# Performance work log

Measured on AMD Instinct MI355X. Metric: run time of the kernel, lower is better.

## Reference

```python
import jax, jax.numpy as jnp
import numpy as np

BATCH, SEQ, DIM = 4, 4096, 256
DT_RANK, D_STATE, NUM_TOKENS = 16, 16, 1024


def _adapool(x, T):
    # uniform window mean == AdaptiveAvgPool1d when S % T == 0
    B, S, D = x.shape
    return x.reshape(B, T, S // T, D).mean(axis=2)


def _layernorm(x, g, b, eps=1e-5):
    mu = x.mean(-1, keepdims=True)
    var = ((x - mu) ** 2).mean(-1, keepdims=True)
    return (x - mu) * jax.lax.rsqrt(var + eps) * g + b


def _gauss_mask(T):
    c = (T + 1) // 2
    idx = jnp.arange(T, dtype=jnp.float32)
    sigma = jnp.abs(idx - c).mean()
    w = jnp.exp(-0.5 * (idx - c) ** 2 / sigma ** 2)
    return w / w.sum()


def _ssm(x, Wdbc, Wdt, bdt, Alog, D):
    A = -jnp.exp(Alog)                                     # (Dm, N)
    dbc = x @ Wdbc.T                                       # (B,L,dt+2N)
    delta = jax.nn.softplus(dbc[..., :DT_RANK] @ Wdt.T + bdt)   # (B,L,Dm)
    Bm = dbc[..., DT_RANK:DT_RANK + D_STATE]               # (B,L,N)
    Cm = dbc[..., DT_RANK + D_STATE:]                      # (B,L,N)
    deltaA = jnp.exp(delta[..., None] * A)                 # (B,L,Dm,N)
    BX = (delta[..., None] * Bm[:, :, None, :]) * x[..., None]
    def comb(c1, c2):
        a1, x1 = c1
        a2, x2 = c2
        return (a2 * a1, a2 * x1 + x2)
    _, hs = jax.lax.associative_scan(comb, (deltaA, BX), axis=1)
    y = jnp.einsum('bldn,bln->bld', hs, Cm) + D * x
    return y


def setup_inputs():
    key = jax.random.key(0)
    ks = jax.random.split(key, 16)
    s = 0.05
    Alog = jnp.tile(jnp.log(jnp.arange(1.0, D_STATE + 1.0, dtype=jnp.float32))[None, :], (DIM, 1))
    return {
        'x': jax.random.normal(ks[0], (BATCH, SEQ, DIM), jnp.float32),
        'ln_g': jnp.ones((DIM,), jnp.float32),
        'ln_b': jnp.zeros((DIM,), jnp.float32),
        'W1': jax.random.normal(ks[1], (DIM, DIM), jnp.float32) * s,
        'b1': jnp.zeros((DIM,), jnp.float32),
        'W2': jax.random.normal(ks[2], (DIM, DIM), jnp.float32) * s,
        'b2': jnp.zeros((DIM,), jnp.float32),
        'Wcf': jax.random.normal(ks[3], (DIM, DIM), jnp.float32) * s,
        'bcf': jnp.zeros((DIM,), jnp.float32),
        'Wcb': jax.random.normal(ks[4], (DIM, DIM), jnp.float32) * s,
        'bcb': jnp.zeros((DIM,), jnp.float32),
        'Wdbc_f': jax.random.normal(ks[5], (DT_RANK + 2 * D_STATE, DIM), jnp.float32) * s,
        'Wdt_f': jax.random.normal(ks[6], (DIM, DT_RANK), jnp.float32) * s,
        'bdt_f': jnp.zeros((DIM,), jnp.float32),
        'Alog_f': Alog,
        'D_f': jnp.ones((DIM,), jnp.float32),
        'Wdbc_b': jax.random.normal(ks[7], (DT_RANK + 2 * D_STATE, DIM), jnp.float32) * s,
        'Wdt_b': jax.random.normal(ks[8], (DIM, DT_RANK), jnp.float32) * s,
        'bdt_b': jnp.zeros((DIM,), jnp.float32),
        'Alog_b': Alog,
        'D_b': jnp.ones((DIM,), jnp.float32),
    }


def reference(x, ln_g, ln_b, W1, b1, W2, b2, Wcf, bcf, Wcb, bcb,
              Wdbc_f, Wdt_f, bdt_f, Alog_f, D_f,
              Wdbc_b, Wdt_b, bdt_b, Alog_b, D_b):
    skip = _adapool(x, NUM_TOKENS)
    xn = _layernorm(x, ln_g, ln_b)
    z = xn @ W1.T + b1
    xp = xn @ W2.T + b2
    mask = _gauss_mask(NUM_TOKENS)[None, :, None]

    # forward direction: 1x1 conv (= channel linear) -> softplus -> SSM
    h1 = jax.nn.softplus(jnp.einsum('bsd,ed->bse', xp, Wcf) + bcf)
    x1 = _ssm(h1, Wdbc_f, Wdt_f, bdt_f, Alog_f, D_f)
    x1 = jax.nn.silu(_adapool(x1, NUM_TOKENS) * mask)

    # backward direction on flipped sequence
    h2 = jax.nn.softplus(jnp.einsum('bsd,ed->bse', xp[:, ::-1], Wcb) + bcb)
    x2 = _ssm(h2, Wdbc_b, Wdt_b, bdt_b, Alog_b, D_b)[:, ::-1]
    x2 = jax.nn.silu(_adapool(x2, NUM_TOKENS) * mask)

    zp = jax.nn.silu(_adapool(z, NUM_TOKENS))
    return zp * x1 + zp * x2 + skip
```

## Files before the change

kernel.cpp:

```cpp
#include <hip/hip_runtime.h>
#include <math.h>


namespace {
constexpr int BB = 4;
constexpr int LL = 4096;
constexpr int DD = 256;
constexpr int NS = 16;
constexpr int NCH = 128;
constexpr int CLEN = 32;
constexpr int NG  = CLEN / 8;
constexpr int TOK = 1024;

constexpr size_t NROW = (size_t)BB * LL;
constexpr size_t NE   = NROW * DD;
constexpr size_t NP   = (size_t)BB * TOK * DD;
constexpr size_t NBC  = NROW * NS;
constexpr size_t NAGG = 2ull * BB * DD * NCH * NS;
constexpr size_t NSD  = 2ull * BB * NCH * DD;

constexpr size_t O_H1X  = 0;
constexpr size_t O_G2X  = NE / 2;
constexpr size_t O_H1T  = NE;
constexpr size_t O_G2T  = NE + NE / 2;
constexpr size_t O_DLTF = 2 * NE;
constexpr size_t O_XN   = O_DLTF;
constexpr size_t O_DLTB = 2 * NE + NE / 2;
constexpr size_t O_BMF  = 3 * NE;
constexpr size_t O_CMF  = O_BMF + NBC / 2;
constexpr size_t O_BMB  = O_CMF + NBC / 2;
constexpr size_t O_CMB  = O_BMB + NBC / 2;
constexpr size_t O_ZP   = O_CMB + NBC / 2;
constexpr size_t O_WF1  = O_ZP + NP;
constexpr size_t O_BF1  = O_WF1 + 768 * 256 / 2;
constexpr size_t O_WF2F = O_BF1 + 768;
constexpr size_t O_B2F  = O_WF2F + 384 * 256 / 2;
constexpr size_t O_WF2B = O_B2F + 384;
constexpr size_t O_B2B  = O_WF2B + 384 * 256 / 2;
constexpr size_t O_SD   = O_B2B + 384;
constexpr size_t O_HEND = O_SD + NSD;
constexpr size_t O_HIN  = O_HEND + NAGG / 2;
constexpr size_t O_MASK = O_HIN + NAGG / 2;

constexpr int SST = 136;
constexpr int NWPREP = 1282;
}

typedef __bf16 bf16x8 __attribute__((ext_vector_type(8)));
typedef __bf16 bf16x4 __attribute__((ext_vector_type(4)));
typedef float f32x4 __attribute__((ext_vector_type(4)));

__device__ __forceinline__ float softplusf(float x) {
    return fmaxf(x, 0.f) + __logf(1.f + __expf(-fabsf(x)));
}
__device__ __forceinline__ float siluf(float x) {
    return x / (1.f + __expf(-x));
}
__device__ __forceinline__ void gl_lds16(const void* g, void* l) {
    __builtin_amdgcn_global_load_lds((const __attribute__((address_space(1))) unsigned int*)g,
                                     (__attribute__((address_space(3))) unsigned int*)l, 16, 0, 0);
}
__device__ __forceinline__ int st_addr(int col, int row) {
    return col * SST + ((((row >> 3) ^ (col >> 3)) & 15) << 3) + (row & 7);
}
__device__ __forceinline__ void pow_chain(float e1, float* p) {
    p[0] = e1;
    p[1] = e1 * e1;
    p[2] = p[1] * e1;
    p[3] = p[1] * p[1];
    p[4] = p[3] * p[0];
    p[5] = p[3] * p[1];
    p[6] = p[3] * p[2];
    p[7] = p[3] * p[3];
    p[8]  = p[7] * p[0];
    p[9]  = p[7] * p[1];
    p[10] = p[7] * p[2];
    p[11] = p[7] * p[3];
    p[12] = p[7] * p[4];
    p[13] = p[7] * p[5];
    p[14] = p[7] * p[6];
    p[15] = p[7] * p[7];
}

#define GEMM_KLOOP(SHBASE, GA, GB, WR, WC, WV, LANE, ACC)                          \
    {                                                                               \
        _Pragma("unroll")                                                           \
        for (int rg = 0; rg < 2; ++rg) {                                            \
            gl_lds16((GA) + rg * 16 * 256, &(SHBASE)[((WV) * 2 + rg) * 512]);       \
            gl_lds16((GB) + rg * 16 * 256, &(SHBASE)[4096 + ((WV) * 2 + rg) * 512]);\
        }                                                                           \
        _Pragma("unroll")                                                           \
        for (int kst = 0; kst < 8; ++kst) {                                         \
            if (kst < 7) {                                                          \
                __bf16* Asn = (SHBASE) + ((kst + 1) & 1) * 8192;                    \
                int k0n = (kst + 1) * 32;                                           \
                _Pragma("unroll")                                                   \
                for (int rg = 0; rg < 2; ++rg) {                                    \
                    gl_lds16((GA) + rg * 16 * 256 + k0n, &Asn[((WV) * 2 + rg) * 512]);      \
                    gl_lds16((GB) + rg * 16 * 256 + k0n, &Asn[4096 + ((WV) * 2 + rg) * 512]);\
                }                                                                   \
                asm volatile("s_waitcnt vmcnt(4)" ::: "memory");                    \
            } else {                                                                \
                asm volatile("s_waitcnt vmcnt(0)" ::: "memory");                    \
            }                                                                       \
            __builtin_amdgcn_s_barrier();                                           \
            __builtin_amdgcn_sched_barrier(0);                                      \
            const __bf16* Ac = (SHBASE) + (kst & 1) * 8192;                         \
            const __bf16* Bc = Ac + 4096;                                           \
            bf16x8 af[4], bfr[4];                                                   \
            _Pragma("unroll")                                                       \
            for (int i = 0; i < 4; ++i)                                             \
                af[i] = *(const bf16x8*)&Ac[((WR) * 4 + i) * 512 + (LANE) * 8];     \
            _Pragma("unroll")                                                       \
            for (int j = 0; j < 4; ++j)                                             \
                bfr[j] = *(const bf16x8*)&Bc[((WC) * 4 + j) * 512 + (LANE) * 8];    \
            _Pragma("unroll")                                                       \
            for (int i = 0; i < 4; ++i)                                             \
                _Pragma("unroll")                                                   \
                for (int j = 0; j < 4; ++j)                                         \
                    ACC[i][j] = __builtin_amdgcn_mfma_f32_16x16x32_bf16(af[i], bfr[j], ACC[i][j], 0, 0, 0); \
            __builtin_amdgcn_s_barrier();                                           \
        }                                                                           \
    }

__global__ __launch_bounds__(256) void prep_ln_kernel(
    const float* __restrict__ x, const float* __restrict__ lng, const float* __restrict__ lnb,
    const float* __restrict__ W1, const float* __restrict__ b1,
    const float* __restrict__ W2, const float* __restrict__ b2,
    const float* __restrict__ Wcf, const float* __restrict__ bcf,
    const float* __restrict__ Wcb, const float* __restrict__ bcb,
    const float* __restrict__ Wdt_f, const float* __restrict__ Wdbc_f, const float* __restrict__ bdt_f,
    const float* __restrict__ Wdt_b, const float* __restrict__ Wdbc_b, const float* __restrict__ bdt_b,
    __bf16* __restrict__ xn, float* __restrict__ outp,
    __bf16* __restrict__ Wf1, float* __restrict__ bf1,
    __bf16* __restrict__ Wf2f, float* __restrict__ b2f,
    __bf16* __restrict__ Wf2b, float* __restrict__ b2b,
    float* __restrict__ mask)
{
    int bxg = blockIdx.x;
    int k = threadIdx.x;
    if (bxg >= NWPREP) {
        __shared__ float ls[4][256];
        int r0 = (bxg - NWPREP) * 4;
        int w = k >> 6, l = k & 63;
        int row = r0 + w;
        float4 v = *(const float4*)&x[(size_t)row * 256 + l * 4];
        float s = v.x + v.y + v.z + v.w;
        float q = v.x * v.x + v.y * v.y + v.z * v.z + v.w * v.w;
        for (int o = 32; o > 0; o >>= 1) {
            s += __shfl_xor(s, o, 64);
            q += __shfl_xor(q, o, 64);
        }
        float mu = s * (1.f / 256.f);
        float rs = rsqrtf(q * (1.f / 256.f) - mu * mu + 1e-5f);
        float4 g4 = *(const float4*)&lng[l * 4];
        float4 b4 = *(const float4*)&lnb[l * 4];
        bf16x4 o4;
        o4[0] = (__bf16)((v.x - mu) * rs * g4.x + b4.x);
        o4[1] = (__bf16)((v.y - mu) * rs * g4.y + b4.y);
        o4[2] = (__bf16)((v.z - mu) * rs * g4.z + b4.z);
        o4[3] = (__bf16)((v.w - mu) * rs * g4.w + b4.w);
        *(bf16x4*)&xn[(size_t)row * 256 + l * 4] = o4;
        *(float4*)&ls[w][l * 4] = v;
        __syncthreads();
        int b = r0 >> 12;
        int g = (r0 & 4095) >> 2;
        float acc = ls[0][k] + ls[1][k] + ls[2][k] + ls[3][k];
        outp[((size_t)b * TOK + g) * 256 + k] = acc * 0.25f;
        return;
    }
    int j2 = bxg;
    int mat = j2 / 641;
    int bx = j2 % 641;
    if (bx < 256) {
        int j = bx;
        const float* Wc = mat ? Wcb : Wcf;
        float acc = 0.f, accb = 0.f;
#pragma unroll 8
        for (int m = 0; m < 256; ++m) {
            float w = Wc[j * 256 + m];
            acc  = fmaf(w, W2[m * 256 + k], acc);
            accb = fmaf(w, b2[m], accb);
        }
        Wf1[(size_t)(256 + mat * 256 + j) * 256 + k] = (__bf16)acc;
        if (k == 0) bf1[256 + mat * 256 + j] = accb + (mat ? bcb[j] : bcf[j]);
        if (mat == 0) {
            Wf1[(size_t)j * 256 + k] = (__bf16)W1[j * 256 + k];
            if (k == 0) bf1[j] = b1[j];
        }
    } else if (bx < 640) {
        int j = bx - 256;
        const float* Wdt  = mat ? Wdt_b : Wdt_f;
        const float* Wdbc = mat ? Wdbc_b : Wdbc_f;
        const float* bdt  = mat ? bdt_b : bdt_f;
        __bf16* Wf2 = mat ? Wf2b : Wf2f;
        float* b2x  = mat ? b2b : b2f;
        float val;
        if (j < 256) {
            float acc = 0.f;
#pragma unroll
            for (int m = 0; m < 16; ++m)
                acc = fmaf(Wdt[j * 16 + m], Wdbc[m * 256 + k], acc);
            val = acc;
        } else if (j < 288) {
            val = Wdbc[(16 + (j - 256)) * 256 + k];
        } else {
            val = 0.f;
        }
        Wf2[(size_t)j * 256 + k] = (__bf16)val;
        if (k == 0) b2x[j] = (j < 256) ? bdt[j] : 0.f;
    } else if (mat == 0) {
        __shared__ float red2[4];
        __shared__ float sb;
        float w[4];
        float loc = 0.f;
#pragma unroll
        for (int q = 0; q < 4; ++q) {
            float dd = (float)(k + 256 * q) - 512.f;
            w[q] = __expf(-0.5f * dd * dd * (1.f / 65536.f));
            loc += w[q];
        }
        for (int o = 32; o > 0; o >>= 1) loc += __shfl_xor(loc, o, 64);
        if ((k & 63) == 0) red2[k >> 6] = loc;
        __syncthreads();
        if (k == 0) sb = red2[0] + red2[1] + red2[2] + red2[3];
        __syncthreads();
        float inv = 1.f / sb;
#pragma unroll
        for (int q = 0; q < 4; ++q) mask[k + 256 * q] = w[q] * inv;
    }
}

__global__ __launch_bounds__(256) void gemm1_mfma(
    const __bf16* __restrict__ A, const __bf16* __restrict__ Bw, const float* __restrict__ bias,
    float* __restrict__ zp, __bf16* __restrict__ h1x, __bf16* __restrict__ g2x,
    __bf16* __restrict__ h1T, __bf16* __restrict__ g2T)
{
    __shared__ __align__(16) __bf16 SH[128 * SST];
    int tid = threadIdx.x;
    int lane = tid & 63, wv = tid >> 6;
    int wr = wv >> 1, wc = wv & 1;
    int lm = lane & 15, lq = lane >> 4;
    int m0 = blockIdx.x << 7, n0 = blockIdx.y << 7;

    const __bf16* gaB = A  + (size_t)(m0 + wv * 32 + lm) * 256 + lq * 8;
    const __bf16* gbB = Bw + (size_t)(n0 + wv * 32 + lm) * 256 + lq * 8;

    f32x4 acc[4][4];
#pragma unroll
    for (int i = 0; i < 4; ++i)
#pragma unroll
        for (int j = 0; j < 4; ++j) acc[i][j] = 0;

    GEMM_KLOOP(SH, gaB, gbB, wr, wc, wv, lane, acc)

    int target = blockIdx.y >> 1;
    int colbase = (blockIdx.y & 1) * 128;
    __syncthreads();
    if (target == 0) {
        float* zs = (float*)SH;
#pragma unroll
        for (int j = 0; j < 4; ++j) {
            int coll = wc * 64 + j * 16 + lm;
            float bv = bias[n0 + coll];
#pragma unroll
            for (int i = 0; i < 4; ++i) {
                int gl = wr * 16 + i * 4 + lq;
                float s = acc[i][j][0] + acc[i][j][1] + acc[i][j][2] + acc[i][j][3];
                zs[gl * 132 + coll] = siluf(0.25f * s + bv);
            }
        }
        __syncthreads();
        int b = m0 >> 12, g0 = (m0 & 4095) >> 2;
        int rl = tid >> 5;
        int c4 = (tid & 31) * 4;
#pragma unroll
        for (int p = 0; p < 4; ++p) {
            int g = p * 8 + rl;
            float4 v = *(float4*)&zs[g * 132 + c4];
            *(float4*)&zp[((size_t)b * TOK + g0 + g) * 256 + colbase + c4] = v;
        }
    } else {
        __bf16* hs = SH;
#pragma unroll
        for (int j = 0; j < 4; ++j) {
            int coll = wc * 64 + j * 16 + lm;
            float bv = bias[n0 + coll];
#pragma unroll
            for (int i = 0; i < 4; ++i) {
                int rl = wr * 64 + i * 16 + lq * 4;
                bf16x4 v4;
#pragma unroll
                for (int r = 0; r < 4; ++r)
                    v4[r] = (__bf16)softplusf(acc[i][j][r] + bv);
                *(bf16x4*)&hs[st_addr(coll, rl)] = v4;
            }
        }
        __syncthreads();
        __bf16* outp = (target == 1) ? h1x : g2x;
        __bf16* outT = (target == 1) ? h1T : g2T;
        {
            int tg = tid >> 4;
#pragma unroll
            for (int it = 0; it < 8; ++it) {
                int dcol = it * 16 + (tid & 15);
                bf16x8 v = *(const bf16x8*)&hs[dcol * SST + (((tg ^ (dcol >> 3)) & 15) << 3)];
                *(bf16x8*)&outT[(((size_t)(m0 >> 3) + tg) * 256 + colbase + dcol) * 8] = v;
            }
        }
        {
            int rl2 = tid >> 4;
            int c8 = (tid & 15) * 8;
#pragma unroll
            for (int p = 0; p < 8; ++p) {
                int row = p * 16 + rl2;
                bf16x8 v;
#pragma unroll
                for (int e = 0; e < 8; ++e) v[e] = hs[st_addr(c8 + e, row)];
                *(bf16x8*)&outp[(size_t)(m0 + row) * 256 + colbase + c8] = v;
            }
        }
    }
}

__global__ __launch_bounds__(256) void gemm2_mfma(
    const __bf16* __restrict__ h1x, const __bf16* __restrict__ g2x,
    const __bf16* __restrict__ Wf, const float* __restrict__ bf2,
    const __bf16* __restrict__ Wb, const float* __restrict__ bb2,
    __bf16* __restrict__ dTf, __bf16* __restrict__ dTb,
    __bf16* __restrict__ BmF, __bf16* __restrict__ CmF,
    __bf16* __restrict__ BmB, __bf16* __restrict__ CmB)
{
    __shared__ __align__(16) __bf16 SH[128 * SST];
    int tid = threadIdx.x;
    int lane = tid & 63, wv = tid >> 6;
    int wr = wv >> 1, wc = wv & 1;
    int lm = lane & 15, lq = lane >> 4;
    int m0 = blockIdx.x << 7, n0 = blockIdx.y << 7;
    int dir = blockIdx.z;
    const __bf16* A    = dir ? g2x : h1x;
    const __bf16* Bw   = dir ? Wb : Wf;
    const float* bias  = dir ? bb2 : bf2;
    __bf16* dT = dir ? dTb : dTf;
    __bf16* Bm = dir ? BmB : BmF;
    __bf16* Cm = dir ? CmB : CmF;

    const __bf16* gaB = A  + (size_t)(m0 + wv * 32 + lm) * 256 + lq * 8;
    const __bf16* gbB = Bw + (size_t)(n0 + wv * 32 + lm) * 256 + lq * 8;

    f32x4 acc[4][4];
#pragma unroll
    for (int i = 0; i < 4; ++i)
#pragma unroll
        for (int j = 0; j < 4; ++j) acc[i][j] = 0;

    GEMM_KLOOP(SH, gaB, gbB, wr, wc, wv, lane, acc)

    __syncthreads();
    if (blockIdx.y < 2) {
        __bf16* hs = SH;
        int colbase = blockIdx.y * 128;
#pragma unroll
        for (int j = 0; j < 4; ++j) {
            int coll = wc * 64 + j * 16 + lm;
            float bv = bias[n0 + coll];
#pragma unroll
            for (int i = 0; i < 4; ++i) {
                int rl = wr * 64 + i * 16 + lq * 4;
                bf16x4 v4;
#pragma unroll
                for (int r = 0; r < 4; ++r)
                    v4[r] = (__bf16)softplusf(acc[i][j][r] + bv);
                *(bf16x4*)&hs[st_addr(coll, rl)] = v4;
            }
        }
        __syncthreads();
        int tg = tid >> 4;
#pragma unroll
        for (int it = 0; it < 8; ++it) {
            int dcol = it * 16 + (tid & 15);
            bf16x8 v = *(const bf16x8*)&hs[dcol * SST + (((tg ^ (dcol >> 3)) & 15) << 3)];
            *(bf16x8*)&dT[(((size_t)(m0 >> 3) + tg) * 256 + colbase + dcol) * 8] = v;
        }
    } else {
        __bf16* bs_ = SH;
        __bf16* cs_ = SH + 128 * 24;
        if (wc == 0) {
#pragma unroll
            for (int j = 0; j < 2; ++j) {
                int coll = j * 16 + lm;
                float bv = bias[n0 + coll];
                __bf16* dst = j ? cs_ : bs_;
#pragma unroll
                for (int i = 0; i < 4; ++i) {
                    int rl = wr * 64 + i * 16 + lq * 4;
#pragma unroll
                    for (int r = 0; r < 4; ++r)
                        dst[(rl + r) * 24 + lm] = (__bf16)(acc[i][j][r] + bv);
                }
            }
        }
        __syncthreads();
        int row = tid >> 1;
        int c8 = (tid & 1) * 8;
        bf16x8 vb = *(bf16x8*)&bs_[row * 24 + c8];
        bf16x8 vc = *(bf16x8*)&cs_[row * 24 + c8];
        *(bf16x8*)&Bm[(size_t)(m0 + row) * 16 + c8] = vb;
        *(bf16x8*)&Cm[(size_t)(m0 + row) * 16 + c8] = vc;
    }
}

__global__ __launch_bounds__(256) void scan1_kernel(
    const __bf16* __restrict__ dTf, const __bf16* __restrict__ dTb,
    const __bf16* __restrict__ xTf, const __bf16* __restrict__ xTb,
    const __bf16* __restrict__ bmf, const __bf16* __restrict__ bmb,
    const float* __restrict__ alogf, const float* __restrict__ alogb,
    float* __restrict__ sdb, __bf16* __restrict__ hend)
{
    int d = threadIdx.x;
    int c = blockIdx.x, b = blockIdx.y, dir = blockIdx.z;
    const __bf16* dT = dir ? dTb : dTf;
    const __bf16* xT = dir ? xTb : xTf;
    const __bf16* Bm = dir ? bmb : bmf;
    const float* Alog = dir ? alogb : alogf;

    float A[16];
    bool intOK = true;
#pragma unroll
    for (int n = 0; n < 16; ++n) {
        A[n] = -__expf(Alog[(size_t)d * 16 + n]);
        intOK = intOK && (fabsf(A[n] + (float)(n + 1)) < 1e-3f);
    }
    float h[16];
#pragma unroll
    for (int n = 0; n < 16; ++n) h[n] = 0.f;
    float sd = 0.f;
    size_t rg0 = (size_t)b * 512 + (size_t)c * NG;
    size_t rowb = (size_t)b * LL + (size_t)c * CLEN;
    if (intOK) {
        for (int g = 0; g < NG; ++g) {
            int gg = dir ? (NG - 1 - g) : g;
            size_t ti = ((rg0 + gg) * 256 + d) * 8;
            bf16x8 dv = *(const bf16x8*)&dT[ti];
            bf16x8 xv8 = *(const bf16x8*)&xT[ti];
#pragma unroll
            for (int ii = 0; ii < 8; ++ii) {
                int i = dir ? (7 - ii) : ii;
                float dlt = (float)dv[i];
                float xv  = (float)xv8[i];
                float common = dlt * xv;
                sd += dlt;
                float p[16];
                pow_chain(__expf(-dlt), p);
                const bf16x8* Bp = (const bf16x8*)&Bm[(rowb + gg * 8 + i) * NS];
                bf16x8 b0 = Bp[0], b1 = Bp[1];
#pragma unroll
                for (int n = 0; n < 8; ++n) {
                    h[n]     = fmaf(p[n],     h[n],     common * (float)b0[n]);
                    h[n + 8] = fmaf(p[n + 8], h[n + 8], common * (float)b1[n]);
                }
            }
        }
    } else {
        for (int g = 0; g < NG; ++g) {
            int gg = dir ? (NG - 1 - g) : g;
            size_t ti = ((rg0 + gg) * 256 + d) * 8;
            bf16x8 dv = *(const bf16x8*)&dT[ti];
            bf16x8 xv8 = *(const bf16x8*)&xT[ti];
#pragma unroll
            for (int ii = 0; ii < 8; ++ii) {
                int i = dir ? (7 - ii) : ii;
                float dlt = (float)dv[i];
                float xv  = (float)xv8[i];
                float common = dlt * xv;
                sd += dlt;
                const bf16x8* Bp = (const bf16x8*)&Bm[(rowb + gg * 8 + i) * NS];
                bf16x8 b0 = Bp[0], b1 = Bp[1];
#pragma unroll
                for (int n = 0; n < 8; ++n) {
                    h[n]     = fmaf(__expf(dlt * A[n]),     h[n],     common * (float)b0[n]);
                    h[n + 8] = fmaf(__expf(dlt * A[n + 8]), h[n + 8], common * (float)b1[n]);
                }
            }
        }
    }
    size_t sbase = (size_t)(dir * 4 + b) * NCH + c;
    sdb[sbase * 256 + d] = sd;
    size_t hb = sbase * 16 * 256 + d;
#pragma unroll
    for (int n = 0; n < 16; ++n) hend[hb + (size_t)n * 256] = (__bf16)h[n];
}

__global__ __launch_bounds__(128) void scan2_kernel(
    const float* __restrict__ sdb, const __bf16* __restrict__ hend,
    const float* __restrict__ alogf, const float* __restrict__ alogb,
    __bf16* __restrict__ hin)
{
    int blk = blockIdx.x >> 1;
    int n = blk & 15, b = (blk >> 4) & 3, dir = blk >> 6;
    int d = ((blockIdx.x & 1) << 7) + threadIdx.x;
    const float* Alog = dir ? alogb : alogf;
    float A_dn = -__expf(Alog[(size_t)d * 16 + n]);
    size_t basec = (size_t)(dir * 4 + b) * NCH;
    float s = 0.f;
    if (!dir) {
#pragma unroll 8
        for (int c = 0; c < NCH; ++c) {
            float sdv = sdb[(basec + c) * 256 + d];
            size_t idx = ((basec + c) * 16 + n) * 256 + d;
            float he = (float)hend[idx];
            hin[idx] = (__bf16)s;
            s = fmaf(__expf(sdv * A_dn), s, he);
        }
    } else {
#pragma unroll 8
        for (int c = NCH - 1; c >= 0; --c) {
            float sdv = sdb[(basec + c) * 256 + d];
            size_t idx = ((basec + c) * 16 + n) * 256 + d;
            float he = (float)hend[idx];
            hin[idx] = (__bf16)s;
            s = fmaf(__expf(sdv * A_dn), s, he);
        }
    }
}

__global__ __launch_bounds__(256) void scan3_kernel(
    const __bf16* __restrict__ dTf, const __bf16* __restrict__ dTb,
    const __bf16* __restrict__ xTf, const __bf16* __restrict__ xTb,
    const __bf16* __restrict__ bmf, const __bf16* __restrict__ bmb,
    const __bf16* __restrict__ cmf, const __bf16* __restrict__ cmb,
    const float* __restrict__ alogf, const float* __restrict__ alogb,
    const float* __restrict__ Dfp, const float* __restrict__ Dbp,
    const __bf16* __restrict__ hin,
    const float* __restrict__ zp, const float* __restrict__ mask,
    float* __restrict__ outp)
{
    int d = threadIdx.x;
    int c = blockIdx.x, b = blockIdx.y, dir = blockIdx.z;
    const __bf16* dT = dir ? dTb : dTf;
    const __bf16* xT = dir ? xTb : xTf;
    const __bf16* Bm = dir ? bmb : bmf;
    const __bf16* Cm = dir ? cmb : cmf;
    const float* Alog = dir ? alogb : alogf;
    const float* Dv   = dir ? Dbp : Dfp;

    float A[16];
    bool intOK = true;
#pragma unroll
    for (int n = 0; n < 16; ++n) {
        A[n] = -__expf(Alog[(size_t)d * 16 + n]);
        intOK = intOK && (fabsf(A[n] + (float)(n + 1)) < 1e-3f);
    }
    float Dd = Dv[d];
    float h[16];
    size_t hb = ((size_t)(dir * 4 + b) * NCH + c) * 16 * 256 + d;
#pragma unroll
    for (int n = 0; n < 16; ++n) h[n] = (float)hin[hb + (size_t)n * 256];

    size_t rg0 = (size_t)b * 512 + (size_t)c * NG;
    size_t rowb = (size_t)b * LL + (size_t)c * CLEN;
    int base = c * CLEN;
    float pool = 0.f;
    if (intOK) {
        for (int g = 0; g < NG; ++g) {
            int gg = dir ? (NG - 1 - g) : g;
            size_t ti = ((rg0 + gg) * 256 + d) * 8;
            bf16x8 dv = *(const bf16x8*)&dT[ti];
            bf16x8 xv8 = *(const bf16x8*)&xT[ti];
#pragma unroll
            for (int ii = 0; ii < 8; ++ii) {
                int i = dir ? (7 - ii) : ii;
                float dlt = (float)dv[i];
                float xv  = (float)xv8[i];
                float common = dlt * xv;
                float p[16];
                pow_chain(__expf(-dlt), p);
                size_t row = rowb + gg * 8 + i;
                const bf16x8* Bp = (const bf16x8*)&Bm[row * NS];
                const bf16x8* Cp = (const bf16x8*)&Cm[row * NS];
                bf16x8 b0 = Bp[0], b1 = Bp[1];
                bf16x8 c0 = Cp[0], c1 = Cp[1];
                float yac = 0.f;
#pragma unroll
                for (int n = 0; n < 8; ++n) {
                    h[n]     = fmaf(p[n],     h[n],     common * (float)b0[n]);
                    h[n + 8] = fmaf(p[n + 8], h[n + 8], common * (float)b1[n]);
                    yac = fmaf(h[n], (float)c0[n], yac);
                    yac = fmaf(h[n + 8], (float)c1[n], yac);
                }
                pool += yac + Dd * xv;
                int t = base + gg * 8 + i;
                bool gend = dir ? ((t & 3) == 0) : ((t & 3) == 3);
                if (gend) {
                    int gtok = t >> 2;
                    size_t ip = ((size_t)b * TOK + gtok) * 256 + d;
                    float contrib = zp[ip] * siluf(pool * 0.25f * mask[gtok]);
                    atomicAdd(&outp[ip], contrib);
                    pool = 0.f;
                }
            }
        }
    } else {
        for (int g = 0; g < NG; ++g) {
            int gg = dir ? (NG - 1 - g) : g;
            size_t ti = ((rg0 + gg) * 256 + d) * 8;
            bf16x8 dv = *(const bf16x8*)&dT[ti];
            bf16x8 xv8 = *(const bf16x8*)&xT[ti];
#pragma unroll
            for (int ii = 0; ii < 8; ++ii) {
                int i = dir ? (7 - ii) : ii;
                float dlt = (float)dv[i];
                float xv  = (float)xv8[i];
                float common = dlt * xv;
                size_t row = rowb + gg * 8 + i;
                const bf16x8* Bp = (const bf16x8*)&Bm[row * NS];
                const bf16x8* Cp = (const bf16x8*)&Cm[row * NS];
                bf16x8 b0 = Bp[0], b1 = Bp[1];
                bf16x8 c0 = Cp[0], c1 = Cp[1];
                float yac = 0.f;
#pragma unroll
                for (int n = 0; n < 8; ++n) {
                    h[n]     = fmaf(__expf(dlt * A[n]),     h[n],     common * (float)b0[n]);
                    h[n + 8] = fmaf(__expf(dlt * A[n + 8]), h[n + 8], common * (float)b1[n]);
                    yac = fmaf(h[n], (float)c0[n], yac);
                    yac = fmaf(h[n + 8], (float)c1[n], yac);
                }
                pool += yac + Dd * xv;
                int t = base + gg * 8 + i;
                bool gend = dir ? ((t & 3) == 0) : ((t & 3) == 3);
                if (gend) {
                    int gtok = t >> 2;
                    size_t ip = ((size_t)b * TOK + gtok) * 256 + d;
                    float contrib = zp[ip] * siluf(pool * 0.25f * mask[gtok]);
                    atomicAdd(&outp[ip], contrib);
                    pool = 0.f;
                }
            }
        }
    }
}

extern "C" void kernel_launch(void* const* d_in, const int* in_sizes, int n_in,
                              void* d_out, int out_size, void* d_ws, size_t ws_size,
                              hipStream_t stream)
{
    const float* x      = (const float*)d_in[0];
    const float* ln_g   = (const float*)d_in[1];
    const float* ln_b   = (const float*)d_in[2];
    const float* W1     = (const float*)d_in[3];
    const float* b1     = (const float*)d_in[4];
    const float* W2     = (const float*)d_in[5];
    const float* b2     = (const float*)d_in[6];
    const float* Wcf    = (const float*)d_in[7];
    const float* bcf    = (const float*)d_in[8];
    const float* Wcb    = (const float*)d_in[9];
    const float* bcb    = (const float*)d_in[10];
    const float* Wdbc_f = (const float*)d_in[11];
    const float* Wdt_f  = (const float*)d_in[12];
    const float* bdt_f  = (const float*)d_in[13];
    const float* Alog_f = (const float*)d_in[14];
    const float* D_f    = (const float*)d_in[15];
    const float* Wdbc_b = (const float*)d_in[16];
    const float* Wdt_b  = (const float*)d_in[17];
    const float* bdt_b  = (const float*)d_in[18];
    const float* Alog_b = (const float*)d_in[19];
    const float* D_b    = (const float*)d_in[20];
    float* out = (float*)d_out;
    float* ws  = (float*)d_ws;

    __bf16* h1x = (__bf16*)(ws + O_H1X);
    __bf16* g2x = (__bf16*)(ws + O_G2X);
    __bf16* h1T = (__bf16*)(ws + O_H1T);
    __bf16* g2T = (__bf16*)(ws + O_G2T);
    __bf16* xnb = (__bf16*)(ws + O_XN);
    __bf16* dTf = (__bf16*)(ws + O_DLTF);
    __bf16* dTb = (__bf16*)(ws + O_DLTB);
    __bf16* bmf = (__bf16*)(ws + O_BMF);
    __bf16* cmf = (__bf16*)(ws + O_CMF);
    __bf16* bmb = (__bf16*)(ws + O_BMB);
    __bf16* cmb = (__bf16*)(ws + O_CMB);
    float* zpb  = ws + O_ZP;
    __bf16* wf1 = (__bf16*)(ws + O_WF1);
    float* bf1  = ws + O_BF1;
    __bf16* wf2f = (__bf16*)(ws + O_WF2F);
    float* b2f  = ws + O_B2F;
    __bf16* wf2b = (__bf16*)(ws + O_WF2B);
    float* b2b  = ws + O_B2B;
    float* sdb  = ws + O_SD;
    __bf16* hnd = (__bf16*)(ws + O_HEND);
    __bf16* hin = (__bf16*)(ws + O_HIN);
    float* mkb  = ws + O_MASK;

    prep_ln_kernel<<<dim3(4096 + NWPREP), 256, 0, stream>>>(
        x, ln_g, ln_b,
        W1, b1, W2, b2, Wcf, bcf, Wcb, bcb,
        Wdt_f, Wdbc_f, bdt_f, Wdt_b, Wdbc_b, bdt_b,
        xnb, out, wf1, bf1, wf2f, b2f, wf2b, b2b, mkb);
    gemm1_mfma<<<dim3(128, 6), 256, 0, stream>>>(xnb, wf1, bf1, zpb, h1x, g2x, h1T, g2T);
    gemm2_mfma<<<dim3(128, 3, 2), 256, 0, stream>>>(h1x, g2x, wf2f, b2f, wf2b, b2b,
                                                    dTf, dTb, bmf, cmf, bmb, cmb);
    scan1_kernel<<<dim3(NCH, BB, 2), 256, 0, stream>>>(dTf, dTb, h1T, g2T, bmf, bmb,
                                                       Alog_f, Alog_b, sdb, hnd);
    scan2_kernel<<<256, 128, 0, stream>>>(sdb, hnd, Alog_f, Alog_b, hin);
    scan3_kernel<<<dim3(NCH, BB, 2), 256, 0, stream>>>(dTf, dTb, h1T, g2T, bmf, bmb, cmf, cmb,
                                                       Alog_f, Alog_b, D_f, D_b, hin,
                                                       zpb, mkb, out);
}
```

Baseline: 207.1 us.

## Merge scan directions into one block and replace atomics with shared-memory reduction

The final scan kernel now runs both the forward and backward directions in a single 512-thread block per chunk and batch. Pooled sums go to shared memory, and after a barrier one half of the threads combines both directions and does a plain read-modify-write to the output. This removes the global atomicAdds and cuts the per-token zp/mask/silu work to one pass. The cost is halving the grid size, adding a block-wide sync, and 16KB of LDS per block, which may reduce occupancy.

Measured after the change: 212.5 us. +2.6%, slower.

```diff
diff --git a/kernel.cpp b/kernel.cpp
--- a/kernel.cpp
+++ b/kernel.cpp
@@ -524,7 +524,7 @@
     }
 }
 
-__global__ __launch_bounds__(256) void scan3_kernel(
+__global__ __launch_bounds__(512) void scan3_kernel(
     const __bf16* __restrict__ dTf, const __bf16* __restrict__ dTb,
     const __bf16* __restrict__ xTf, const __bf16* __restrict__ xTb,
     const __bf16* __restrict__ bmf, const __bf16* __restrict__ bmb,
@@ -535,8 +535,11 @@
     const float* __restrict__ zp, const float* __restrict__ mask,
     float* __restrict__ outp)
 {
-    int d = threadIdx.x;
-    int c = blockIdx.x, b = blockIdx.y, dir = blockIdx.z;
+    __shared__ float ls[4096];
+    int tid = threadIdx.x;
+    int d = tid & 255;
+    int dir = tid >> 8;
+    int c = blockIdx.x, b = blockIdx.y;
     const __bf16* dT = dir ? dTb : dTf;
     const __bf16* xT = dir ? xTb : xTf;
     const __bf16* Bm = dir ? bmb : bmf;
@@ -592,10 +595,8 @@
                 int t = base + gg * 8 + i;
                 bool gend = dir ? ((t & 3) == 0) : ((t & 3) == 3);
                 if (gend) {
-                    int gtok = t >> 2;
-                    size_t ip = ((size_t)b * TOK + gtok) * 256 + d;
-                    float contrib = zp[ip] * siluf(pool * 0.25f * mask[gtok]);
-                    atomicAdd(&outp[ip], contrib);
+                    int gl = (t >> 2) - (c << 3);
+                    ls[(dir << 11) + (gl << 8) + d] = pool;
                     pool = 0.f;
                 }
             }
@@ -629,13 +630,24 @@
                 int t = base + gg * 8 + i;
                 bool gend = dir ? ((t & 3) == 0) : ((t & 3) == 3);
                 if (gend) {
-                    int gtok = t >> 2;
-                    size_t ip = ((size_t)b * TOK + gtok) * 256 + d;
-                    float contrib = zp[ip] * siluf(pool * 0.25f * mask[gtok]);
-                    atomicAdd(&outp[ip], contrib);
+                    int gl = (t >> 2) - (c << 3);
+                    ls[(dir << 11) + (gl << 8) + d] = pool;
                     pool = 0.f;
                 }
             }
+        }
+    }
+    __syncthreads();
+    if (tid < 256) {
+        int gtok0 = c << 3;
+        size_t ipb = ((size_t)b * TOK + gtok0) * 256 + tid;
+#pragma unroll
+        for (int gl = 0; gl < 8; ++gl) {
+            float mk = mask[gtok0 + gl] * 0.25f;
+            float zv = zp[ipb + (size_t)gl * 256];
+            float pf = ls[(gl << 8) + tid];
+            float pb = ls[2048 + (gl << 8) + tid];
+            outp[ipb + (size_t)gl * 256] += zv * (siluf(pf * mk) + siluf(pb * mk));
         }
     }
 }
@@ -702,7 +714,7 @@
     scan1_kernel<<<dim3(NCH, BB, 2), 256, 0, stream>>>(dTf, dTb, h1T, g2T, bmf, bmb,
                                                        Alog_f, Alog_b, sdb, hnd);
     scan2_kernel<<<256, 128, 0, stream>>>(sdb, hnd, Alog_f, Alog_b, hin);
-    scan3_kernel<<<dim3(NCH, BB, 2), 256, 0, stream>>>(dTf, dTb, h1T, g2T, bmf, bmb, cmf, cmb,
-                                                       Alog_f, Alog_b, D_f, D_b, hin,
-                                                       zpb, mkb, out);
-}
+    scan3_kernel<<<dim3(NCH, BB), 512, 0, stream>>>(dTf, dTb, h1T, g2T, bmf, bmb, cmf, cmb,
+                                                    Alog_f, Alog_b, D_f, D_b, hin,
+                                                    zpb, mkb, out);
+}
```
